# Kernel tuning notes

Measured on AMD Instinct MI355X. Metric: run time of the kernel, lower is better.

The kernel has to match this reference:

```python
import jax, jax.numpy as jnp
import numpy as np

HIDDEN = 2048
NUM_EXPERTS = 64
TOP_K = 8
EPS = 1e-6


def setup_inputs() -> dict:
    key = jax.random.key(0)
    k1, k2, k3, k4 = jax.random.split(key, 4)
    hidden_states = jax.random.normal(k1, (4, 4096, HIDDEN), dtype=jnp.float32)
    scale = jnp.ones((HIDDEN,), dtype=jnp.float32) + 0.01 * jax.random.normal(k2, (HIDDEN,), dtype=jnp.float32)
    proj_w = jax.random.normal(k3, (NUM_EXPERTS, HIDDEN), dtype=jnp.float32) * (HIDDEN ** -0.5)
    per_expert_scale = jnp.ones((NUM_EXPERTS,), dtype=jnp.float32) + 0.01 * jax.random.normal(k4, (NUM_EXPERTS,), dtype=jnp.float32)
    return {"hidden_states": hidden_states, "scale": scale, "proj_w": proj_w, "per_expert_scale": per_expert_scale}


def reference(hidden_states, scale, proj_w, per_expert_scale):
    H = hidden_states.shape[-1]
    # RMSNorm without learned scale
    x = hidden_states * jax.lax.rsqrt(jnp.mean(hidden_states * hidden_states, axis=-1, keepdims=True) + EPS)
    # elementwise scale and 1/sqrt(H) root-size scaling
    x = x * scale * (H ** -0.5)
    # router logits: [B,S,E]
    logits = jnp.einsum("bsh,eh->bse", x, proj_w)
    router_probs = jax.nn.softmax(logits.astype(jnp.float32), axis=-1)
    top_k_weights, top_k_index = jax.lax.top_k(router_probs, TOP_K)
    top_k_weights = top_k_weights / jnp.sum(top_k_weights, axis=-1, keepdims=True)
    top_k_weights = top_k_weights * per_expert_scale[top_k_index]
    # histc with bins=E, min=0, max=E on integer indices == bincount
    num_tokens_per_expert = jnp.bincount(top_k_index.reshape(-1), length=NUM_EXPERTS).astype(jnp.float32)
    return (top_k_weights.astype(hidden_states.dtype), top_k_index, num_tokens_per_expert)
```

## Files before the change

kernel.cpp:

```cpp
#include <hip/hip_runtime.h>
#include <math.h>

#define HIDDEN   2048
#define NEXPERT  64
#define TOPK     8
#define NTOK     16384
#define TOKB     16
#define CHUNK    256
#define NCHUNK   8
#define ROWP     264
#define RSQRT_H  0.02209708691207961
#define WSCALE   64.0f

typedef __attribute__((ext_vector_type(8))) _Float16 v8h;
typedef __attribute__((ext_vector_type(4))) float    v4f;

static __device__ __forceinline__ unsigned short f16b(float x) {
    return __builtin_bit_cast(unsigned short, (_Float16)x);
}
static __device__ __forceinline__ float f16f(unsigned short u) {
    return (float)__builtin_bit_cast(_Float16, u);
}

__global__ __launch_bounds__(256) void prep_wf(
    const float* __restrict__ w, const float* __restrict__ scale,
    unsigned short* __restrict__ wf)
{
    int i    = blockIdx.x * 256 + threadIdx.x;
    int j    = i & 7;
    int lane = (i >> 3) & 63;
    int nt   = (i >> 9) & 3;
    int ks   = i >> 11;
    int e    = nt * 16 + (lane & 15);
    int k    = ks * 32 + (lane >> 4) * 8 + j;
    float v  = w[e * HIDDEN + k] * scale[k] * WSCALE;
    unsigned short vh = f16b(v);
    unsigned short vl = f16b(v - f16f(vh));
    size_t base = (((size_t)(ks * 4 + nt) * 2) * 64 + lane) * 8 + j;
    wf[base]       = vh;
    wf[base + 512] = vl;
}

__global__ __launch_bounds__(256, 4) void router_main(
    const float* __restrict__ h, const unsigned short* __restrict__ wf,
    const float* __restrict__ pes,
    float* __restrict__ out_w, float* __restrict__ out_i, float* __restrict__ out_c)
{
    __shared__ __align__(16) char smem[34112];
    unsigned short* Xb0 = (unsigned short*)smem;
    float* lss = (float*)(smem + 33792);
    int*   hist = (int*)(smem + 33856);
    float* lg  = (float*)smem;

    const int tid  = (int)threadIdx.x;
    const int w    = __builtin_amdgcn_readfirstlane(tid >> 6);
    const int lane = tid & 63;
    const int m    = lane & 15;
    const int quad = lane >> 4;
    const int t0   = (int)blockIdx.x * TOKB;

    if (tid < NEXPERT) hist[tid] = 0;

    const int aoff = m * ROWP + quad * 8;

    v4f acc[4];
#pragma unroll
    for (int nt = 0; nt < 4; ++nt) acc[nt] = (v4f)0.f;
    float ss[4] = {0.f, 0.f, 0.f, 0.f};
    float4 st[4];

#pragma unroll
    for (int i = 0; i < 4; ++i) {
        int idx = i * 256 + tid, t = idx >> 6, kq = idx & 63;
        st[i] = *(const float4*)(h + (size_t)(t0 + t) * HIDDEN + kq * 4);
    }
#pragma unroll
    for (int i = 0; i < 4; ++i) {
        int idx = i * 256 + tid, t = idx >> 6, kq = idx & 63;
        float4 v = st[i];
        ss[i] = fmaf(v.x, v.x, fmaf(v.y, v.y, fmaf(v.z, v.z, fmaf(v.w, v.w, ss[i]))));
        unsigned short h0 = f16b(v.x), h1 = f16b(v.y), h2 = f16b(v.z), h3 = f16b(v.w);
        unsigned short l0 = f16b(v.x - f16f(h0)), l1 = f16b(v.y - f16f(h1));
        unsigned short l2 = f16b(v.z - f16f(h2)), l3 = f16b(v.w - f16f(h3));
        uint2 hp = make_uint2((unsigned)h0 | ((unsigned)h1 << 16),
                              (unsigned)h2 | ((unsigned)h3 << 16));
        uint2 lp = make_uint2((unsigned)l0 | ((unsigned)l1 << 16),
                              (unsigned)l2 | ((unsigned)l3 << 16));
        *(uint2*)(&Xb0[t * ROWP + kq * 4])        = hp;
        *(uint2*)(&Xb0[4224 + t * ROWP + kq * 4]) = lp;
    }

    for (int c = 0; c < NCHUNK; ++c) {
        __syncthreads();
        unsigned short* buf = Xb0 + (c & 1) * 8448;
        unsigned short* nbuf = Xb0 + ((c + 1) & 1) * 8448;

        if (c < NCHUNK - 1) {
#pragma unroll
            for (int i = 0; i < 4; ++i) {
                int idx = i * 256 + tid, t = idx >> 6, kq = idx & 63;
                st[i] = *(const float4*)(h + (size_t)(t0 + t) * HIDDEN
                                           + (c + 1) * CHUNK + kq * 4);
            }
        }

#pragma unroll
        for (int s = 0; s < 2; ++s) {
            const int ksl = 2 * w + s;
            const int ksg = c * 8 + ksl;
            v8h ah = *(const v8h*)(&buf[aoff + ksl * 32]);
            v8h al = *(const v8h*)(&buf[4224 + aoff + ksl * 32]);
#pragma unroll
            for (int nt = 0; nt < 4; ++nt) {
                const unsigned short* bp =
                    wf + (((size_t)(ksg * 4 + nt) * 2) * 64 + lane) * 8;
                v8h bh = *(const v8h*)bp;
                v8h bl = *(const v8h*)(bp + 512);
                acc[nt] = __builtin_amdgcn_mfma_f32_16x16x32_f16(ah, bh, acc[nt], 0, 0, 0);
                acc[nt] = __builtin_amdgcn_mfma_f32_16x16x32_f16(ah, bl, acc[nt], 0, 0, 0);
                acc[nt] = __builtin_amdgcn_mfma_f32_16x16x32_f16(al, bh, acc[nt], 0, 0, 0);
            }
        }

        if (c < NCHUNK - 1) {
#pragma unroll
            for (int i = 0; i < 4; ++i) {
                int idx = i * 256 + tid, t = idx >> 6, kq = idx & 63;
                float4 v = st[i];
                ss[i] = fmaf(v.x, v.x, fmaf(v.y, v.y, fmaf(v.z, v.z, fmaf(v.w, v.w, ss[i]))));
                unsigned short h0 = f16b(v.x), h1 = f16b(v.y), h2 = f16b(v.z), h3 = f16b(v.w);
                unsigned short l0 = f16b(v.x - f16f(h0)), l1 = f16b(v.y - f16f(h1));
                unsigned short l2 = f16b(v.z - f16f(h2)), l3 = f16b(v.w - f16f(h3));
                uint2 hp = make_uint2((unsigned)h0 | ((unsigned)h1 << 16),
                                      (unsigned)h2 | ((unsigned)h3 << 16));
                uint2 lp = make_uint2((unsigned)l0 | ((unsigned)l1 << 16),
                                      (unsigned)l2 | ((unsigned)l3 << 16));
                *(uint2*)(&nbuf[t * ROWP + kq * 4])        = hp;
                *(uint2*)(&nbuf[4224 + t * ROWP + kq * 4]) = lp;
            }
        }
    }

#pragma unroll
    for (int i = 0; i < 4; ++i) {
        float s = ss[i];
#pragma unroll
        for (int off = 32; off; off >>= 1) s += __shfl_xor(s, off, 64);
        if (lane == 0) lss[i * 4 + w] = s;
    }
    __syncthreads();

#pragma unroll
    for (int nt = 0; nt < 4; ++nt)
#pragma unroll
        for (int r = 0; r < 4; ++r) {
            int tl = quad * 4 + r;
            lg[(w * 16 + tl) * 65 + nt * 16 + m] = acc[nt][r];
        }
    __syncthreads();

    for (int i = 0; i < 4; ++i) {
        const int tok = w * 4 + i;
        float lsum = (lg[tok * 65 + lane]          + lg[1040 + tok * 65 + lane])
                   + (lg[2080 + tok * 65 + lane]   + lg[3120 + tok * 65 + lane]);
        double sst = (double)lss[tok];
        double rr  = 1.0 / sqrt(sst * (1.0 / (double)HIDDEN) + 1e-6);
        float logit = (float)((double)lsum * rr * (RSQRT_H / (double)WSCALE));

        float work = logit;
        float myval = 0.f; int myidx = 0; float m0 = 0.f;
#pragma unroll
        for (int j = 0; j < TOPK; ++j) {
            float mx = work;
#pragma unroll
            for (int off = 32; off; off >>= 1) mx = fmaxf(mx, __shfl_xor(mx, off, 64));
            unsigned long long msk = __ballot(work == mx);
            int src = __ffsll((long long)msk) - 1;
            if (j == 0) m0 = mx;
            if (lane == j) { myval = mx; myidx = src; }
            if (lane == src) work = -3.402823466e38f;
        }

        float ev = (lane < TOPK) ? expf(myval - m0) : 0.f;
        float es = ev;
        es += __shfl_xor(es, 1, 64);
        es += __shfl_xor(es, 2, 64);
        es += __shfl_xor(es, 4, 64);
        if (lane < TOPK) {
            float wgt = (ev / es) * pes[myidx];
            size_t o = (size_t)(t0 + tok) * TOPK + lane;
            out_w[o] = wgt;
            out_i[o] = (float)myidx;
            atomicAdd(&hist[myidx], 1);
        }
    }

    __syncthreads();
    if (tid < NEXPERT)
        atomicAdd(&out_c[tid], (float)hist[tid]);
}

extern "C" void kernel_launch(void* const* d_in, const int* in_sizes, int n_in,
                              void* d_out, int out_size, void* d_ws, size_t ws_size,
                              hipStream_t stream) {
    const float* h     = (const float*)d_in[0];
    const float* scale = (const float*)d_in[1];
    const float* w     = (const float*)d_in[2];
    const float* pes   = (const float*)d_in[3];

    unsigned short* wf = (unsigned short*)d_ws;

    float* out_w = (float*)d_out;
    float* out_i = (float*)d_out + (size_t)NTOK * TOPK;
    float* out_c = (float*)d_out + (size_t)NTOK * TOPK * 2;

    hipMemsetAsync(out_c, 0, NEXPERT * sizeof(float), stream);

    prep_wf<<<512, 256, 0, stream>>>(w, scale, wf);

    router_main<<<NTOK / TOKB, 256, 0, stream>>>(h, wf, pes, out_w, out_i, out_c);
}
```

Measured before the change: 234.1 us.

## Load activations directly into MFMA registers, split K across 8 waves

The router kernel no longer stages hidden states through double-buffered LDS. Each lane now loads its own fp32 A-fragment from global memory, splits it into hi/lo fp16 in registers, and feeds the MFMAs directly. The block grows to 512 threads, with 8 waves each covering a 256-wide K slice, and partial logits and sums of squares are reduced across waves in LDS. The separate memset is folded into the prep kernel to drop one launch. The cost is uncoalesced 32-byte strided global reads in place of coalesced chunk loads, plus a larger cross-wave reduction.

```diff
diff --git a/kernel.cpp b/kernel.cpp
--- a/kernel.cpp
+++ b/kernel.cpp
@@ -6,14 +6,12 @@
 #define TOPK     8
 #define NTOK     16384
 #define TOKB     16
-#define CHUNK    256
-#define NCHUNK   8
-#define ROWP     264
 #define RSQRT_H  0.02209708691207961
 #define WSCALE   64.0f
 
-typedef __attribute__((ext_vector_type(8))) _Float16 v8h;
-typedef __attribute__((ext_vector_type(4))) float    v4f;
+typedef __attribute__((ext_vector_type(8))) _Float16       v8h;
+typedef __attribute__((ext_vector_type(8))) unsigned short v8u;
+typedef __attribute__((ext_vector_type(4))) float          v4f;
 
 static __device__ __forceinline__ unsigned short f16b(float x) {
     return __builtin_bit_cast(unsigned short, (_Float16)x);
@@ -24,9 +22,10 @@
 
 __global__ __launch_bounds__(256) void prep_wf(
     const float* __restrict__ w, const float* __restrict__ scale,
-    unsigned short* __restrict__ wf)
+    unsigned short* __restrict__ wf, float* __restrict__ out_c)
 {
     int i    = blockIdx.x * 256 + threadIdx.x;
+    if (i < NEXPERT) out_c[i] = 0.f;
     int j    = i & 7;
     int lane = (i >> 3) & 63;
     int nt   = (i >> 9) & 3;
@@ -41,16 +40,14 @@
     wf[base + 512] = vl;
 }
 
-__global__ __launch_bounds__(256, 4) void router_main(
+__global__ __launch_bounds__(512, 8) void router_main(
     const float* __restrict__ h, const unsigned short* __restrict__ wf,
     const float* __restrict__ pes,
     float* __restrict__ out_w, float* __restrict__ out_i, float* __restrict__ out_c)
 {
-    __shared__ __align__(16) char smem[34112];
-    unsigned short* Xb0 = (unsigned short*)smem;
-    float* lss = (float*)(smem + 33792);
-    int*   hist = (int*)(smem + 33856);
-    float* lg  = (float*)smem;
+    __shared__ __align__(16) float lg[8 * 16 * 65];
+    __shared__ float lss[8 * 16];
+    __shared__ int   hist[NEXPERT];
 
     const int tid  = (int)threadIdx.x;
     const int w    = __builtin_amdgcn_readfirstlane(tid >> 6);
@@ -61,109 +58,73 @@
 
     if (tid < NEXPERT) hist[tid] = 0;
 
-    const int aoff = m * ROWP + quad * 8;
+    const float* xp = h + (size_t)(t0 + m) * HIDDEN + w * 256 + quad * 8;
+    const unsigned short* wq = wf + (size_t)(w * 8) * 4096 + (size_t)lane * 8;
 
     v4f acc[4];
 #pragma unroll
     for (int nt = 0; nt < 4; ++nt) acc[nt] = (v4f)0.f;
-    float ss[4] = {0.f, 0.f, 0.f, 0.f};
-    float4 st[4];
+    float ssl = 0.f;
 
+    float4 xa = *(const float4*)xp;
+    float4 xb = *(const float4*)(xp + 4);
+
+    for (int i = 0; i < 8; ++i) {
+        float vv[8] = {xa.x, xa.y, xa.z, xa.w, xb.x, xb.y, xb.z, xb.w};
+        if (i < 7) {
+            xa = *(const float4*)(xp + (i + 1) * 32);
+            xb = *(const float4*)(xp + (i + 1) * 32 + 4);
+        }
+        v8u uh, ul;
 #pragma unroll
-    for (int i = 0; i < 4; ++i) {
-        int idx = i * 256 + tid, t = idx >> 6, kq = idx & 63;
-        st[i] = *(const float4*)(h + (size_t)(t0 + t) * HIDDEN + kq * 4);
-    }
+        for (int j = 0; j < 8; ++j) {
+            float v = vv[j];
+            unsigned short hh = f16b(v);
+            uh[j] = hh;
+            ul[j] = f16b(v - f16f(hh));
+            ssl   = fmaf(v, v, ssl);
+        }
+        v8h ah = __builtin_bit_cast(v8h, uh);
+        v8h al = __builtin_bit_cast(v8h, ul);
+
+        const unsigned short* bq = wq + (size_t)i * 4096;
 #pragma unroll
-    for (int i = 0; i < 4; ++i) {
-        int idx = i * 256 + tid, t = idx >> 6, kq = idx & 63;
-        float4 v = st[i];
-        ss[i] = fmaf(v.x, v.x, fmaf(v.y, v.y, fmaf(v.z, v.z, fmaf(v.w, v.w, ss[i]))));
-        unsigned short h0 = f16b(v.x), h1 = f16b(v.y), h2 = f16b(v.z), h3 = f16b(v.w);
-        unsigned short l0 = f16b(v.x - f16f(h0)), l1 = f16b(v.y - f16f(h1));
-        unsigned short l2 = f16b(v.z - f16f(h2)), l3 = f16b(v.w - f16f(h3));
-        uint2 hp = make_uint2((unsigned)h0 | ((unsigned)h1 << 16),
-                              (unsigned)h2 | ((unsigned)h3 << 16));
-        uint2 lp = make_uint2((unsigned)l0 | ((unsigned)l1 << 16),
-                              (unsigned)l2 | ((unsigned)l3 << 16));
-        *(uint2*)(&Xb0[t * ROWP + kq * 4])        = hp;
-        *(uint2*)(&Xb0[4224 + t * ROWP + kq * 4]) = lp;
-    }
-
-    for (int c = 0; c < NCHUNK; ++c) {
-        __syncthreads();
-        unsigned short* buf = Xb0 + (c & 1) * 8448;
-        unsigned short* nbuf = Xb0 + ((c + 1) & 1) * 8448;
-
-        if (c < NCHUNK - 1) {
-#pragma unroll
-            for (int i = 0; i < 4; ++i) {
-                int idx = i * 256 + tid, t = idx >> 6, kq = idx & 63;
-                st[i] = *(const float4*)(h + (size_t)(t0 + t) * HIDDEN
-                                           + (c + 1) * CHUNK + kq * 4);
-            }
-        }
-
-#pragma unroll
-        for (int s = 0; s < 2; ++s) {
-            const int ksl = 2 * w + s;
-            const int ksg = c * 8 + ksl;
-            v8h ah = *(const v8h*)(&buf[aoff + ksl * 32]);
-            v8h al = *(const v8h*)(&buf[4224 + aoff + ksl * 32]);
-#pragma unroll
-            for (int nt = 0; nt < 4; ++nt) {
-                const unsigned short* bp =
-                    wf + (((size_t)(ksg * 4 + nt) * 2) * 64 + lane) * 8;
-                v8h bh = *(const v8h*)bp;
-                v8h bl = *(const v8h*)(bp + 512);
-                acc[nt] = __builtin_amdgcn_mfma_f32_16x16x32_f16(ah, bh, acc[nt], 0, 0, 0);
-                acc[nt] = __builtin_amdgcn_mfma_f32_16x16x32_f16(ah, bl, acc[nt], 0, 0, 0);
-                acc[nt] = __builtin_amdgcn_mfma_f32_16x16x32_f16(al, bh, acc[nt], 0, 0, 0);
-            }
-        }
-
-        if (c < NCHUNK - 1) {
-#pragma unroll
-            for (int i = 0; i < 4; ++i) {
-                int idx = i * 256 + tid, t = idx >> 6, kq = idx & 63;
-                float4 v = st[i];
-                ss[i] = fmaf(v.x, v.x, fmaf(v.y, v.y, fmaf(v.z, v.z, fmaf(v.w, v.w, ss[i]))));
-                unsigned short h0 = f16b(v.x), h1 = f16b(v.y), h2 = f16b(v.z), h3 = f16b(v.w);
-                unsigned short l0 = f16b(v.x - f16f(h0)), l1 = f16b(v.y - f16f(h1));
-                unsigned short l2 = f16b(v.z - f16f(h2)), l3 = f16b(v.w - f16f(h3));
-                uint2 hp = make_uint2((unsigned)h0 | ((unsigned)h1 << 16),
-                                      (unsigned)h2 | ((unsigned)h3 << 16));
-                uint2 lp = make_uint2((unsigned)l0 | ((unsigned)l1 << 16),
-                                      (unsigned)l2 | ((unsigned)l3 << 16));
-                *(uint2*)(&nbuf[t * ROWP + kq * 4])        = hp;
-                *(uint2*)(&nbuf[4224 + t * ROWP + kq * 4]) = lp;
-            }
+        for (int nt = 0; nt < 4; ++nt) {
+            const unsigned short* bp = bq + nt * 1024;
+            v8h bh = *(const v8h*)bp;
+            v8h bl = *(const v8h*)(bp + 512);
+            acc[nt] = __builtin_amdgcn_mfma_f32_16x16x32_f16(ah, bh, acc[nt], 0, 0, 0);
+            acc[nt] = __builtin_amdgcn_mfma_f32_16x16x32_f16(ah, bl, acc[nt], 0, 0, 0);
+            acc[nt] = __builtin_amdgcn_mfma_f32_16x16x32_f16(al, bh, acc[nt], 0, 0, 0);
         }
     }
 
-#pragma unroll
-    for (int i = 0; i < 4; ++i) {
-        float s = ss[i];
-#pragma unroll
-        for (int off = 32; off; off >>= 1) s += __shfl_xor(s, off, 64);
-        if (lane == 0) lss[i * 4 + w] = s;
+    {
+        float s = ssl;
+        s += __shfl_xor(s, 16, 64);
+        s += __shfl_xor(s, 32, 64);
+        if (lane < 16) lss[w * 16 + lane] = s;
     }
-    __syncthreads();
 
 #pragma unroll
     for (int nt = 0; nt < 4; ++nt)
 #pragma unroll
-        for (int r = 0; r < 4; ++r) {
-            int tl = quad * 4 + r;
-            lg[(w * 16 + tl) * 65 + nt * 16 + m] = acc[nt][r];
-        }
+        for (int r = 0; r < 4; ++r)
+            lg[(w * 16 + quad * 4 + r) * 65 + nt * 16 + m] = acc[nt][r];
+
     __syncthreads();
 
-    for (int i = 0; i < 4; ++i) {
-        const int tok = w * 4 + i;
-        float lsum = (lg[tok * 65 + lane]          + lg[1040 + tok * 65 + lane])
-                   + (lg[2080 + tok * 65 + lane]   + lg[3120 + tok * 65 + lane]);
-        double sst = (double)lss[tok];
+    for (int i = 0; i < 2; ++i) {
+        const int tok = w * 2 + i;
+        float lsum = ((lg[(0 * 16 + tok) * 65 + lane] + lg[(1 * 16 + tok) * 65 + lane])
+                    + (lg[(2 * 16 + tok) * 65 + lane] + lg[(3 * 16 + tok) * 65 + lane]))
+                   + ((lg[(4 * 16 + tok) * 65 + lane] + lg[(5 * 16 + tok) * 65 + lane])
+                    + (lg[(6 * 16 + tok) * 65 + lane] + lg[(7 * 16 + tok) * 65 + lane]));
+        float s01 = lss[0 * 16 + tok] + lss[1 * 16 + tok];
+        float s23 = lss[2 * 16 + tok] + lss[3 * 16 + tok];
+        float s45 = lss[4 * 16 + tok] + lss[5 * 16 + tok];
+        float s67 = lss[6 * 16 + tok] + lss[7 * 16 + tok];
+        double sst = (double)((s01 + s23) + (s45 + s67));
         double rr  = 1.0 / sqrt(sst * (1.0 / (double)HIDDEN) + 1e-6);
         float logit = (float)((double)lsum * rr * (RSQRT_H / (double)WSCALE));
 
@@ -214,9 +175,7 @@
     float* out_i = (float*)d_out + (size_t)NTOK * TOPK;
     float* out_c = (float*)d_out + (size_t)NTOK * TOPK * 2;
 
-    hipMemsetAsync(out_c, 0, NEXPERT * sizeof(float), stream);
+    prep_wf<<<512, 256, 0, stream>>>(w, scale, wf, out_c);
 
-    prep_wf<<<512, 256, 0, stream>>>(w, scale, wf);
-
-    router_main<<<NTOK / TOKB, 256, 0, stream>>>(h, wf, pes, out_w, out_i, out_c);
+    router_main<<<NTOK / TOKB, 512, 0, stream>>>(h, wf, pes, out_w, out_i, out_c);
 }
```

Result: no change. 236.1 us (+0.8%).
